# Kernel optimization log

Hardware: AMD Instinct MI355X
Metric: run time of the kernel (lower is better)

## Reference

```python
import jax, jax.numpy as jnp
import numpy as np

D_MODEL, H, D_K, D_V = 1024, 16, 64, 64
B, N = 8, 1024
EPS = 1e-9

def _xavier(key, shape):
    fan_in, fan_out = shape[1], shape[0]
    limit = float(np.sqrt(6.0 / (fan_in + fan_out)))
    return jax.random.uniform(key, shape, jnp.float32, -limit, limit)

def setup_inputs() -> dict:
    key = jax.random.key(0)
    ks = jax.random.split(key, 9)
    return {
        "queries": jax.random.normal(ks[0], (B, N, D_MODEL), jnp.float32),
        "keys":    jax.random.normal(ks[1], (B, N, D_MODEL), jnp.float32),
        "values":  jax.random.normal(ks[2], (B, N, D_MODEL), jnp.float32),
        "Wq": _xavier(ks[3], (H * D_K, D_MODEL)), "bq": jnp.zeros((H * D_K,), jnp.float32),
        "Wk": _xavier(ks[4], (H * D_K, D_MODEL)), "bk": jnp.zeros((H * D_K,), jnp.float32),
        "Wv": _xavier(ks[5], (H * D_V, D_MODEL)), "bv": jnp.zeros((H * D_V,), jnp.float32),
        "Wo": _xavier(ks[6], (D_MODEL, H * D_V)), "bo": jnp.zeros((D_MODEL,), jnp.float32),
        "Wb": _xavier(ks[7], (D_MODEL, D_MODEL)),  # bilinear weight[0]
        "bb": jnp.zeros((1,), jnp.float32),
        "lambda_param": jnp.asarray(1.0, jnp.float32),
    }

def reference(queries, keys, values, Wq, bq, Wk, bk, Wv, bv, Wo, bo, Wb, bb, lambda_param):
    b_s, nq, _ = queries.shape
    nk = keys.shape[1]
    # QKV projections -> [b, h, n, d]
    q = (queries @ Wq.T + bq).reshape(b_s, nq, H, D_K).transpose(0, 2, 1, 3)
    k = (keys    @ Wk.T + bk).reshape(b_s, nk, H, D_K).transpose(0, 2, 1, 3)
    v = (values  @ Wv.T + bv).reshape(b_s, nk, H, D_V).transpose(0, 2, 1, 3)
    att = jnp.einsum('bhqd,bhkd->bhqk', q, k) / jnp.sqrt(jnp.float32(D_K))
    # Phrasal scores: sigmoid(x W x^T + b), shape [b, nq, nq]
    xW = queries @ Wb  # [b, nq, d_model]
    P = jax.nn.sigmoid(jnp.einsum('bqd,bkd->bqk', xW, queries) + bb[0])
    att = att + lambda_param * jnp.log(P + EPS)[:, None, :, :]
    att = jax.nn.softmax(att, axis=-1)
    out = jnp.einsum('bhqk,bhkd->bhqd', att, v).transpose(0, 2, 1, 3).reshape(b_s, nq, H * D_V)
    out = out @ Wo.T + bo
    return (out, att, P)
```

## Files before the change

### kernel.cpp

```cpp
#include <hip/hip_runtime.h>
#include <cmath>


typedef _Float16 f16;
typedef _Float16 f16x8 __attribute__((ext_vector_type(8)));
typedef _Float16 f16x4 __attribute__((ext_vector_type(4)));
typedef float    f32x4 __attribute__((ext_vector_type(4)));

#define DEVI __device__ __forceinline__

DEVI void async16(const void* g, void* l) {
    __builtin_amdgcn_global_load_lds((const __attribute__((address_space(1))) unsigned int*)g,
                                     (__attribute__((address_space(3))) unsigned int*)l,
                                     16, 0, 0);
}


__global__ __launch_bounds__(256) void cast_qkv(
        const float* __restrict__ q, const float* __restrict__ k, const float* __restrict__ v,
        f16* __restrict__ qh, f16* __restrict__ ql, f16* __restrict__ kh, f16* __restrict__ vh)
{
    size_t i = ((size_t)blockIdx.x * 256 + threadIdx.x) * 4;
    f32x4 qv = *(const f32x4*)(q + i);
    f32x4 kv = *(const f32x4*)(k + i);
    f32x4 vv = *(const f32x4*)(v + i);
    f16x4 a, b, c, d;
#pragma unroll
    for (int j = 0; j < 4; ++j) {
        f16 h = (f16)qv[j];
        a[j] = h;
        b[j] = (f16)(qv[j] - (float)h);
        c[j] = (f16)kv[j];
        d[j] = (f16)vv[j];
    }
    *(f16x4*)(qh + i) = a;
    *(f16x4*)(ql + i) = b;
    *(f16x4*)(kh + i) = c;
    *(f16x4*)(vh + i) = d;
}

__global__ __launch_bounds__(256) void cast_w(
        const float* __restrict__ w0, const float* __restrict__ w1,
        const float* __restrict__ w2, const float* __restrict__ w3,
        f16* __restrict__ o0, f16* __restrict__ o1, f16* __restrict__ o2, f16* __restrict__ o3)
{
    size_t i = ((size_t)blockIdx.x * 256 + threadIdx.x) * 4;
    f32x4 a = *(const f32x4*)(w0 + i);
    f32x4 b = *(const f32x4*)(w1 + i);
    f32x4 c = *(const f32x4*)(w2 + i);
    f32x4 d = *(const f32x4*)(w3 + i);
    f16x4 ra, rb, rc, rd;
#pragma unroll
    for (int j = 0; j < 4; ++j) { ra[j] = (f16)a[j]; rb[j] = (f16)b[j]; rc[j] = (f16)c[j]; rd[j] = (f16)d[j]; }
    *(f16x4*)(o0 + i) = ra;
    *(f16x4*)(o1 + i) = rb;
    *(f16x4*)(o2 + i) = rc;
    *(f16x4*)(o3 + i) = rd;
}

__global__ __launch_bounds__(256) void wb_trans(const float* __restrict__ Wb,
                                                f16* __restrict__ Th, f16* __restrict__ Tl)
{
    __shared__ float tile[64][65];
    const int to = blockIdx.x, td = blockIdx.y, t = threadIdx.x;
#pragma unroll
    for (int it = 0; it < 16; ++it) {
        int e = it * 256 + t;
        int d = e >> 6, o = e & 63;
        tile[o][d] = Wb[(size_t)(td * 64 + d) * 1024 + to * 64 + o];
    }
    __syncthreads();
#pragma unroll
    for (int it = 0; it < 16; ++it) {
        int e = it * 256 + t;
        int o = e >> 6, d = e & 63;
        float v = tile[o][d];
        f16 h = (f16)v;
        size_t idx = (size_t)(to * 64 + o) * 1024 + td * 64 + d;
        Th[idx] = h;
        Tl[idx] = (f16)(v - (float)h);
    }
}

__global__ __launch_bounds__(256) void v_trans(const f16* __restrict__ Vb, f16* __restrict__ Vt)
{
    __shared__ f16 tile[64][72];
    const int nt = blockIdx.x, bh = blockIdx.y, t = threadIdx.x;
    const int b = bh >> 4, h = bh & 15;
#pragma unroll
    for (int it = 0; it < 16; ++it) {
        int e = it * 256 + t;
        int n = e >> 6, d = e & 63;
        tile[d][n] = Vb[((size_t)(b * 1024 + nt * 64 + n)) * 1024 + h * 64 + d];
    }
    __syncthreads();
#pragma unroll
    for (int it = 0; it < 16; ++it) {
        int e = it * 256 + t;
        int d = e >> 6, n = e & 63;
        Vt[((size_t)bh * 64 + d) * 1024 + nt * 64 + n] = tile[d][n];
    }
}

template<int MODE>
__global__ __launch_bounds__(256) void gemm_nt(
        const f16* __restrict__ A, const f16* __restrict__ B,
        const float* __restrict__ bias, void* __restrict__ Cout,
        int M, int N, int K, size_t sA, size_t sB, size_t sC)
{
    __shared__ __align__(16) f16 As[128 * 64];
    __shared__ __align__(16) f16 Bs[128 * 64];
    const int tid = threadIdx.x;
    const int lane = tid & 63;
    const int w = tid >> 6;
    const int wq = w >> 1, wn = w & 1;
    const int l15 = lane & 15, q4 = lane >> 4;
    const size_t z = blockIdx.z;
    const f16* Ab = A + z * sA;
    const f16* Bb = B + z * sB;
    const int tm = blockIdx.y * 128, tn = blockIdx.x * 128;
    const int srow = tid >> 3;
    const int scol = ((tid & 7) ^ (srow & 7)) << 3;

    f32x4 acc[4][4] = {};

    for (int k0 = 0; k0 < K; k0 += 64) {
#pragma unroll
        for (int c = 0; c < 4; ++c) {
            int r = (c << 5) + srow;
            async16(Ab + (size_t)(tm + r) * K + k0 + scol, &As[c * 2048 + tid * 8]);
            async16(Bb + (size_t)(tn + r) * K + k0 + scol, &Bs[c * 2048 + tid * 8]);
        }
        __syncthreads();
#pragma unroll
        for (int ks = 0; ks < 2; ++ks) {
            f16x8 af[4], bf[4];
#pragma unroll
            for (int i = 0; i < 4; ++i) {
                int m = wq * 64 + i * 16 + l15;
                af[i] = *(const f16x8*)&As[m * 64 + ((((ks << 2) + q4) ^ (m & 7)) << 3)];
                int n = wn * 64 + i * 16 + l15;
                bf[i] = *(const f16x8*)&Bs[n * 64 + ((((ks << 2) + q4) ^ (n & 7)) << 3)];
            }
#pragma unroll
            for (int mi = 0; mi < 4; ++mi)
#pragma unroll
                for (int ni = 0; ni < 4; ++ni)
                    acc[mi][ni] = __builtin_amdgcn_mfma_f32_16x16x32_f16(af[mi], bf[ni], acc[mi][ni], 0, 0, 0);
        }
        __syncthreads();
    }

#pragma unroll
    for (int mi = 0; mi < 4; ++mi)
#pragma unroll
        for (int ni = 0; ni < 4; ++ni) {
            const int col = tn + wn * 64 + ni * 16 + l15;
            const float bv = bias[col];
#pragma unroll
            for (int r = 0; r < 4; ++r) {
                const int row = tm + wq * 64 + mi * 16 + q4 * 4 + r;
                const float v = acc[mi][ni][r] + bv;
                const size_t idx = z * sC + (size_t)row * N + col;
                if (MODE == 0) ((float*)Cout)[idx] = v;
                else           ((f16*)Cout)[idx] = (f16)v;
            }
        }
}

template<int MODE>
__global__ __launch_bounds__(256) void gemm_nt3(
        const f16* __restrict__ Ah, const f16* __restrict__ Al,
        const f16* __restrict__ Bh, const f16* __restrict__ Bl,
        void* __restrict__ out0, void* __restrict__ out1,
        const float* __restrict__ bbp, const float* __restrict__ lamp,
        int M, int N, int K, size_t sA, size_t sB, size_t sC)
{
    __shared__ __align__(16) f16 Ash[128 * 32], Asl[128 * 32], Bsh[128 * 32], Bsl[128 * 32];
    const int tid = threadIdx.x;
    const int lane = tid & 63;
    const int w = tid >> 6;
    const int wq = w >> 1, wn = w & 1;
    const int l15 = lane & 15, q4 = lane >> 4;
    const size_t z = blockIdx.z;
    const f16* Ahb = Ah + z * sA; const f16* Alb = Al + z * sA;
    const f16* Bhb = Bh + z * sB; const f16* Blb = Bl + z * sB;
    const int tm = blockIdx.y * 128, tn = blockIdx.x * 128;
    const int srow = tid >> 2;
    const int scol = ((tid & 3) ^ (srow & 3)) << 3;

    f32x4 acc[4][4] = {};

    for (int k0 = 0; k0 < K; k0 += 32) {
#pragma unroll
        for (int c = 0; c < 2; ++c) {
            int r = (c << 6) + srow;
            const size_t ga = (size_t)(tm + r) * K + k0 + scol;
            const size_t gb = (size_t)(tn + r) * K + k0 + scol;
            async16(Ahb + ga, &Ash[c * 2048 + tid * 8]);
            async16(Alb + ga, &Asl[c * 2048 + tid * 8]);
            async16(Bhb + gb, &Bsh[c * 2048 + tid * 8]);
            async16(Blb + gb, &Bsl[c * 2048 + tid * 8]);
        }
        __syncthreads();
        f16x8 ah[4], al[4], bh[4], bl[4];
#pragma unroll
        for (int i = 0; i < 4; ++i) {
            int m = wq * 64 + i * 16 + l15;
            int offa = m * 32 + ((q4 ^ (m & 3)) << 3);
            ah[i] = *(const f16x8*)&Ash[offa];
            al[i] = *(const f16x8*)&Asl[offa];
            int n = wn * 64 + i * 16 + l15;
            int offb = n * 32 + ((q4 ^ (n & 3)) << 3);
            bh[i] = *(const f16x8*)&Bsh[offb];
            bl[i] = *(const f16x8*)&Bsl[offb];
        }
#pragma unroll
        for (int mi = 0; mi < 4; ++mi)
#pragma unroll
            for (int ni = 0; ni < 4; ++ni) {
                acc[mi][ni] = __builtin_amdgcn_mfma_f32_16x16x32_f16(ah[mi], bh[ni], acc[mi][ni], 0, 0, 0);
                acc[mi][ni] = __builtin_amdgcn_mfma_f32_16x16x32_f16(ah[mi], bl[ni], acc[mi][ni], 0, 0, 0);
                acc[mi][ni] = __builtin_amdgcn_mfma_f32_16x16x32_f16(al[mi], bh[ni], acc[mi][ni], 0, 0, 0);
            }
        __syncthreads();
    }

    float bb0 = 0.f, l8 = 0.f;
    if constexpr (MODE == 1) { bb0 = bbp[0]; l8 = 8.f * lamp[0]; }
#pragma unroll
    for (int mi = 0; mi < 4; ++mi)
#pragma unroll
        for (int ni = 0; ni < 4; ++ni) {
            const int row0 = tm + wq * 64 + mi * 16 + q4 * 4;
            const int col = tn + wn * 64 + ni * 16 + l15;
            if constexpr (MODE == 0) {
#pragma unroll
                for (int r = 0; r < 4; ++r) {
                    const size_t idx = z * sC + (size_t)(row0 + r) * N + col;
                    float v = acc[mi][ni][r];
                    f16 hi = (f16)v;
                    ((f16*)out0)[idx] = hi;
                    ((f16*)out1)[idx] = (f16)(v - (float)hi);
                }
            } else {
                f32x4 lpv;
#pragma unroll
                for (int r = 0; r < 4; ++r) {
                    float zt = acc[mi][ni][r] + bb0;
                    zt = fminf(fmaxf(zt, -87.f), 87.f);
                    float Pv = 1.f / (1.f + expf(-zt));
                    ((float*)out0)[z * sC + (size_t)(row0 + r) * N + col] = Pv;
                    lpv[r] = l8 * logf(Pv + 1e-9f);
                }
                *(f32x4*)&((float*)out1)[z * sC + (size_t)(row0 >> 2) * 4096 + (size_t)col * 4] = lpv;
            }
        }
}

__global__ __launch_bounds__(256) void attn_pass1(
        const f16* __restrict__ Qf, const f16* __restrict__ Kf,
        const float* __restrict__ Lp, float* __restrict__ linv)
{
    __shared__ __align__(16) f16 Ks[2][128 * 64];

    const int qt = blockIdx.x, h = blockIdx.y, b = blockIdx.z;
    const int tid = threadIdx.x, lane = tid & 63, w = tid >> 6;
    const int l15 = lane & 15, q4 = lane >> 4;

    f16x8 aq[2][2];
    const size_t qbase = ((size_t)(b * 1024 + qt * 128 + w * 32)) * 1024 + h * 64;
#pragma unroll
    for (int mi = 0; mi < 2; ++mi)
#pragma unroll
        for (int ks = 0; ks < 2; ++ks)
            aq[mi][ks] = *(const f16x8*)&Qf[qbase + (size_t)(mi * 16 + l15) * 1024 + ks * 32 + q4 * 8];

    const size_t kgbase = ((size_t)b * 1024) * 1024 + h * 64;
    const int srow = tid >> 3;
    const int scol = ((tid & 7) ^ (srow & 7)) << 3;
    const size_t lpb = (size_t)b * 1048576 + (size_t)(qt * 32 + w * 8 + q4) * 4096;

    float lsum[8];
#pragma unroll
    for (int i = 0; i < 8; ++i) lsum[i] = 0.f;

#pragma unroll
    for (int c = 0; c < 4; ++c) {
        int r = (c << 5) + srow;
        async16(&Kf[kgbase + (size_t)r * 1024 + scol], &Ks[0][c * 2048 + tid * 8]);
    }
    __syncthreads();

    int cur = 0;
    for (int kt = 0; kt < 8; ++kt) {
        if (kt < 7) {
#pragma unroll
            for (int c = 0; c < 4; ++c) {
                int r = (c << 5) + srow;
                async16(&Kf[kgbase + (size_t)((kt + 1) * 128 + r) * 1024 + scol],
                        &Ks[cur ^ 1][c * 2048 + tid * 8]);
            }
        }
        f32x4 sc[2][8];
#pragma unroll
        for (int mi = 0; mi < 2; ++mi)
#pragma unroll
            for (int ni = 0; ni < 8; ++ni)
                sc[mi][ni] = *(const f32x4*)&Lp[lpb + (size_t)mi * 16384 +
                                                (size_t)(kt * 128 + ni * 16 + l15) * 4];
#pragma unroll
        for (int ks = 0; ks < 2; ++ks)
#pragma unroll
            for (int ni = 0; ni < 8; ++ni) {
                int n = ni * 16 + l15;
                f16x8 bf = *(const f16x8*)&Ks[cur][n * 64 + ((((ks << 2) + q4) ^ (n & 7)) << 3)];
#pragma unroll
                for (int mi = 0; mi < 2; ++mi)
                    sc[mi][ni] = __builtin_amdgcn_mfma_f32_16x16x32_f16(aq[mi][ks], bf, sc[mi][ni], 0, 0, 0);
            }
#pragma unroll
        for (int mi = 0; mi < 2; ++mi)
#pragma unroll
            for (int r2 = 0; r2 < 4; ++r2) {
                float s = 0.f;
#pragma unroll
                for (int ni = 0; ni < 8; ++ni) s += __expf(sc[mi][ni][r2] * 0.125f);
                lsum[mi * 4 + r2] += s;
            }
        __syncthreads();
        cur ^= 1;
    }

#pragma unroll
    for (int i = 0; i < 8; ++i) {
        float s = lsum[i];
        s += __shfl_xor(s, 1, 16);
        s += __shfl_xor(s, 2, 16);
        s += __shfl_xor(s, 4, 16);
        s += __shfl_xor(s, 8, 16);
        lsum[i] = s;
    }
    if (l15 == 0) {
        const size_t ob = ((size_t)(b * 16 + h)) * 1024 + qt * 128 + w * 32;
#pragma unroll
        for (int mi = 0; mi < 2; ++mi)
#pragma unroll
            for (int r2 = 0; r2 < 4; ++r2)
                linv[ob + mi * 16 + q4 * 4 + r2] = 1.f / lsum[mi * 4 + r2];
    }
}

__global__ __launch_bounds__(256) void attn_pass2(
        const f16* __restrict__ Qf, const f16* __restrict__ Kf,
        const f16* __restrict__ Vt, const float* __restrict__ Lp,
        const float* __restrict__ linv,
        float* __restrict__ att, f16* __restrict__ Obf)
{
    __shared__ __align__(16) f16 Ks[128 * 64];
    __shared__ __align__(16) f16 Vs[64 * 128];
    __shared__ __align__(16) f16 atts[4][32 * 32];

    const int qt = blockIdx.x, h = blockIdx.y, b = blockIdx.z;
    const int tid = threadIdx.x, lane = tid & 63, w = tid >> 6;
    const int l15 = lane & 15, q4 = lane >> 4;

    f16x8 aq[2][2];
    const size_t qbase = ((size_t)(b * 1024 + qt * 128 + w * 32)) * 1024 + h * 64;
#pragma unroll
    for (int mi = 0; mi < 2; ++mi)
#pragma unroll
        for (int ks = 0; ks < 2; ++ks)
            aq[mi][ks] = *(const f16x8*)&Qf[qbase + (size_t)(mi * 16 + l15) * 1024 + ks * 32 + q4 * 8];

    float inv_l[8];
    {
        const size_t lb = ((size_t)(b * 16 + h)) * 1024 + qt * 128 + w * 32;
        f32x4 iv0 = *(const f32x4*)&linv[lb + q4 * 4];
        f32x4 iv1 = *(const f32x4*)&linv[lb + 16 + q4 * 4];
#pragma unroll
        for (int r = 0; r < 4; ++r) { inv_l[r] = iv0[r]; inv_l[4 + r] = iv1[r]; }
    }

    const size_t kgbase = ((size_t)b * 1024) * 1024 + h * 64;
    const size_t lpb = (size_t)b * 1048576 + (size_t)(qt * 32 + w * 8 + q4) * 4096;
    const size_t attbase = ((size_t)((b * 16 + h) * 1024 + qt * 128 + w * 32)) * 1024;
    const int srow = tid >> 3;
    const int scol = ((tid & 7) ^ (srow & 7)) << 3;
    const int vr0 = tid >> 4;
    const int vcb = ((tid & 15) ^ vr0) << 3;

    f32x4 oacc[2][4] = {};
    f16* atts_w = &atts[w][0];

    for (int kt = 0; kt < 8; ++kt) {
#pragma unroll
        for (int c = 0; c < 4; ++c) {
            int r = (c << 5) + srow;
            async16(&Kf[kgbase + (size_t)(kt * 128 + r) * 1024 + scol], &Ks[c * 2048 + tid * 8]);
            int vr = (c << 4) + vr0;
            async16(&Vt[((size_t)(b * 16 + h) * 64 + vr) * 1024 + kt * 128 + vcb], &Vs[c * 2048 + tid * 8]);
        }
        __syncthreads();
#pragma unroll
        for (int qx = 0; qx < 4; ++qx) {
            f32x4 sc[2][2];
#pragma unroll
            for (int mi = 0; mi < 2; ++mi)
#pragma unroll
                for (int nq = 0; nq < 2; ++nq)
                    sc[mi][nq] = *(const f32x4*)&Lp[lpb + (size_t)mi * 16384 +
                                  (size_t)(kt * 128 + qx * 32 + nq * 16 + l15) * 4];
#pragma unroll
            for (int ks = 0; ks < 2; ++ks)
#pragma unroll
                for (int nq = 0; nq < 2; ++nq) {
                    int n = qx * 32 + nq * 16 + l15;
                    f16x8 bf = *(const f16x8*)&Ks[n * 64 + ((((ks << 2) + q4) ^ (n & 7)) << 3)];
#pragma unroll
                    for (int mi = 0; mi < 2; ++mi)
                        sc[mi][nq] = __builtin_amdgcn_mfma_f32_16x16x32_f16(aq[mi][ks], bf, sc[mi][nq], 0, 0, 0);
                }
#pragma unroll
            for (int mi = 0; mi < 2; ++mi)
#pragma unroll
                for (int r2 = 0; r2 < 4; ++r2) {
                    const int ri = mi * 4 + r2;
                    const int qrl = mi * 16 + q4 * 4 + r2;
                    float* attq = &att[attbase + (size_t)qrl * 1024 + kt * 128 + qx * 32];
#pragma unroll
                    for (int nq = 0; nq < 2; ++nq) {
                        const int lc = nq * 16 + l15;
                        float a = __expf(sc[mi][nq][r2] * 0.125f) * inv_l[ri];
                        attq[lc] = a;
                        atts_w[qrl * 32 + (((lc >> 3) ^ ((qrl >> 1) & 3)) << 3) + (lc & 7)] = (f16)a;
                    }
                }
            f16x8 av[2];
#pragma unroll
            for (int mi = 0; mi < 2; ++mi) {
                int m = mi * 16 + l15;
                av[mi] = *(const f16x8*)&atts_w[m * 32 + ((q4 ^ ((m >> 1) & 3)) << 3)];
            }
#pragma unroll
            for (int nv = 0; nv < 4; ++nv) {
                int n = nv * 16 + l15;
                f16x8 bv = *(const f16x8*)&Vs[n * 128 + (((qx * 4 + q4) ^ (n & 15)) << 3)];
#pragma unroll
                for (int mi = 0; mi < 2; ++mi)
                    oacc[mi][nv] = __builtin_amdgcn_mfma_f32_16x16x32_f16(av[mi], bv, oacc[mi][nv], 0, 0, 0);
            }
        }
        __syncthreads();
    }

#pragma unroll
    for (int mi = 0; mi < 2; ++mi)
#pragma unroll
        for (int nv = 0; nv < 4; ++nv)
#pragma unroll
            for (int r2 = 0; r2 < 4; ++r2) {
                const size_t row = (size_t)(b * 1024 + qt * 128 + w * 32 + mi * 16 + q4 * 4 + r2);
                Obf[row * 1024 + h * 64 + nv * 16 + l15] = (f16)oacc[mi][nv][r2];
            }
}


extern "C" void kernel_launch(void* const* d_in, const int* in_sizes, int n_in,
                              void* d_out, int out_size, void* d_ws, size_t ws_size,
                              hipStream_t stream)
{
    (void)in_sizes; (void)n_in; (void)out_size; (void)ws_size;

    const float* queries = (const float*)d_in[0];
    const float* keys    = (const float*)d_in[1];
    const float* values  = (const float*)d_in[2];
    const float* Wq = (const float*)d_in[3];
    const float* bq = (const float*)d_in[4];
    const float* Wk = (const float*)d_in[5];
    const float* bk = (const float*)d_in[6];
    const float* Wv = (const float*)d_in[7];
    const float* bv = (const float*)d_in[8];
    const float* Wo = (const float*)d_in[9];
    const float* bo = (const float*)d_in[10];
    const float* Wb = (const float*)d_in[11];
    const float* bb = (const float*)d_in[12];
    const float* lam = (const float*)d_in[13];

    float* out  = (float*)d_out;
    float* attO = out + (size_t)8 * 1024 * 1024;
    float* POut = attO + (size_t)8 * 16 * 1024 * 1024;

    char* ws = (char*)d_ws;
    const size_t MB = 1024 * 1024;
    f16*  q_hi = (f16*)(ws + 0 * MB);
    f16*  q_lo = (f16*)(ws + 16 * MB);
    f16*  k_h  = (f16*)(ws + 32 * MB);
    f16*  v_h  = (f16*)(ws + 48 * MB);
    f16*  Qb   = (f16*)(ws + 64 * MB);
    f16*  Kb   = (f16*)(ws + 80 * MB);
    f16*  Vt   = (f16*)(ws + 96 * MB);
    float* Lp  = (float*)(ws + 112 * MB);
    f16*  Vb   = (f16*)(ws + 112 * MB);
    f16*  cWq  = (f16*)(ws + 144 * MB);
    f16*  cWk  = cWq + 1024 * 1024;
    f16*  cWv  = cWk + 1024 * 1024;
    f16*  cWo  = cWv + 1024 * 1024;
    f16*  Wbt_h = cWo + 1024 * 1024;
    f16*  Wbt_l = Wbt_h + 1024 * 1024;
    f16*  xw_h = k_h;
    f16*  xw_l = v_h;
    f16*  Obf  = q_lo;
    float* linv = (float*)q_hi;

    const size_t S1M = (size_t)1024 * 1024;

    cast_qkv<<<8192, 256, 0, stream>>>(queries, keys, values, q_hi, q_lo, k_h, v_h);
    cast_w<<<1024, 256, 0, stream>>>(Wq, Wk, Wv, Wo, cWq, cWk, cWv, cWo);
    wb_trans<<<dim3(16, 16), 256, 0, stream>>>(Wb, Wbt_h, Wbt_l);

    gemm_nt<1><<<dim3(8, 64), 256, 0, stream>>>(q_hi, cWq, bq, Qb, 8192, 1024, 1024, 0, 0, 0);
    gemm_nt<1><<<dim3(8, 64), 256, 0, stream>>>(k_h,  cWk, bk, Kb, 8192, 1024, 1024, 0, 0, 0);
    gemm_nt<1><<<dim3(8, 64), 256, 0, stream>>>(v_h,  cWv, bv, Vb, 8192, 1024, 1024, 0, 0, 0);
    v_trans<<<dim3(16, 128), 256, 0, stream>>>(Vb, Vt);

    gemm_nt3<0><<<dim3(8, 64), 256, 0, stream>>>(q_hi, q_lo, Wbt_h, Wbt_l,
                                                 xw_h, xw_l, nullptr, nullptr,
                                                 8192, 1024, 1024, 0, 0, 0);
    gemm_nt3<1><<<dim3(8, 8, 8), 256, 0, stream>>>(xw_h, xw_l, q_hi, q_lo,
                                                   POut, Lp, bb, lam,
                                                   1024, 1024, 1024, S1M, S1M, S1M);

    attn_pass1<<<dim3(8, 16, 8), 256, 0, stream>>>(Qb, Kb, Lp, linv);
    attn_pass2<<<dim3(8, 16, 8), 256, 0, stream>>>(Qb, Kb, Vt, Lp, linv, attO, Obf);

    gemm_nt<0><<<dim3(8, 64), 256, 0, stream>>>(Obf, cWo, bo, out, 8192, 1024, 1024, 0, 0, 0);
}
```

Baseline: 1.119 ms.

## Restructure split-precision GEMMs into segmented passes and tune attention exponentials

The three-term hi/lo split GEMM (hi*hi + hi*lo + lo*hi) is reorganised into three sequential K segments, each streaming one A/B pair through a single 64-wide LDS tile. This halves LDS traffic per step and uses a wider XOR swizzle. The sigmoid and log now use fast intrinsics. The attention passes switch to exp2 with a prescaled constant, and the 1/l normaliser is folded into the exponent as a log2 offset. s_setprio is raised around the MFMA blocks to favour matrix issue. The fast math approximations and the log2 fold can slightly change numerical accuracy.

```diff
diff --git a/kernel.cpp b/kernel.cpp
--- a/kernel.cpp
+++ b/kernel.cpp
@@ -8,6 +8,8 @@
 typedef float    f32x4 __attribute__((ext_vector_type(4)));
 
 #define DEVI __device__ __forceinline__
+
+#define C_EXP2 0.18033688011112042f
 
 DEVI void async16(const void* g, void* l) {
     __builtin_amdgcn_global_load_lds((const __attribute__((address_space(1))) unsigned int*)g,
@@ -169,61 +171,58 @@
 }
 
 template<int MODE>
-__global__ __launch_bounds__(256) void gemm_nt3(
-        const f16* __restrict__ Ah, const f16* __restrict__ Al,
-        const f16* __restrict__ Bh, const f16* __restrict__ Bl,
+__global__ __launch_bounds__(256) void gemm_ntseg(
+        const f16* __restrict__ A0, const f16* __restrict__ A1, const f16* __restrict__ A2,
+        const f16* __restrict__ B0, const f16* __restrict__ B1, const f16* __restrict__ B2,
         void* __restrict__ out0, void* __restrict__ out1,
         const float* __restrict__ bbp, const float* __restrict__ lamp,
-        int M, int N, int K, size_t sA, size_t sB, size_t sC)
-{
-    __shared__ __align__(16) f16 Ash[128 * 32], Asl[128 * 32], Bsh[128 * 32], Bsl[128 * 32];
+        int N, size_t sA, size_t sB, size_t sC)
+{
+    __shared__ __align__(16) f16 As[128 * 64];
+    __shared__ __align__(16) f16 Bs[128 * 64];
     const int tid = threadIdx.x;
     const int lane = tid & 63;
     const int w = tid >> 6;
     const int wq = w >> 1, wn = w & 1;
     const int l15 = lane & 15, q4 = lane >> 4;
     const size_t z = blockIdx.z;
-    const f16* Ahb = Ah + z * sA; const f16* Alb = Al + z * sA;
-    const f16* Bhb = Bh + z * sB; const f16* Blb = Bl + z * sB;
     const int tm = blockIdx.y * 128, tn = blockIdx.x * 128;
-    const int srow = tid >> 2;
-    const int scol = ((tid & 3) ^ (srow & 3)) << 3;
+    const int srow = tid >> 3;
+    const int scol = ((tid & 7) ^ (srow & 7)) << 3;
 
     f32x4 acc[4][4] = {};
 
-    for (int k0 = 0; k0 < K; k0 += 32) {
-#pragma unroll
-        for (int c = 0; c < 2; ++c) {
-            int r = (c << 6) + srow;
-            const size_t ga = (size_t)(tm + r) * K + k0 + scol;
-            const size_t gb = (size_t)(tn + r) * K + k0 + scol;
-            async16(Ahb + ga, &Ash[c * 2048 + tid * 8]);
-            async16(Alb + ga, &Asl[c * 2048 + tid * 8]);
-            async16(Bhb + gb, &Bsh[c * 2048 + tid * 8]);
-            async16(Blb + gb, &Bsl[c * 2048 + tid * 8]);
-        }
-        __syncthreads();
-        f16x8 ah[4], al[4], bh[4], bl[4];
-#pragma unroll
-        for (int i = 0; i < 4; ++i) {
-            int m = wq * 64 + i * 16 + l15;
-            int offa = m * 32 + ((q4 ^ (m & 3)) << 3);
-            ah[i] = *(const f16x8*)&Ash[offa];
-            al[i] = *(const f16x8*)&Asl[offa];
-            int n = wn * 64 + i * 16 + l15;
-            int offb = n * 32 + ((q4 ^ (n & 3)) << 3);
-            bh[i] = *(const f16x8*)&Bsh[offb];
-            bl[i] = *(const f16x8*)&Bsl[offb];
-        }
-#pragma unroll
-        for (int mi = 0; mi < 4; ++mi)
-#pragma unroll
-            for (int ni = 0; ni < 4; ++ni) {
-                acc[mi][ni] = __builtin_amdgcn_mfma_f32_16x16x32_f16(ah[mi], bh[ni], acc[mi][ni], 0, 0, 0);
-                acc[mi][ni] = __builtin_amdgcn_mfma_f32_16x16x32_f16(ah[mi], bl[ni], acc[mi][ni], 0, 0, 0);
-                acc[mi][ni] = __builtin_amdgcn_mfma_f32_16x16x32_f16(al[mi], bh[ni], acc[mi][ni], 0, 0, 0);
-            }
-        __syncthreads();
+#pragma unroll 1
+    for (int seg = 0; seg < 3; ++seg) {
+        const f16* Ab = (seg == 0 ? A0 : (seg == 1 ? A1 : A2)) + z * sA;
+        const f16* Bb = (seg == 0 ? B0 : (seg == 1 ? B1 : B2)) + z * sB;
+#pragma unroll 1
+        for (int k0 = 0; k0 < 1024; k0 += 64) {
+#pragma unroll
+            for (int c = 0; c < 4; ++c) {
+                int r = (c << 5) + srow;
+                async16(Ab + (size_t)(tm + r) * 1024 + k0 + scol, &As[c * 2048 + tid * 8]);
+                async16(Bb + (size_t)(tn + r) * 1024 + k0 + scol, &Bs[c * 2048 + tid * 8]);
+            }
+            __syncthreads();
+#pragma unroll
+            for (int ks = 0; ks < 2; ++ks) {
+                f16x8 af[4], bf[4];
+#pragma unroll
+                for (int i = 0; i < 4; ++i) {
+                    int m = wq * 64 + i * 16 + l15;
+                    af[i] = *(const f16x8*)&As[m * 64 + ((((ks << 2) + q4) ^ (m & 7)) << 3)];
+                    int n = wn * 64 + i * 16 + l15;
+                    bf[i] = *(const f16x8*)&Bs[n * 64 + ((((ks << 2) + q4) ^ (n & 7)) << 3)];
+                }
+#pragma unroll
+                for (int mi = 0; mi < 4; ++mi)
+#pragma unroll
+                    for (int ni = 0; ni < 4; ++ni)
+                        acc[mi][ni] = __builtin_amdgcn_mfma_f32_16x16x32_f16(af[mi], bf[ni], acc[mi][ni], 0, 0, 0);
+            }
+            __syncthreads();
+        }
     }
 
     float bb0 = 0.f, l8 = 0.f;
@@ -249,9 +248,9 @@
                 for (int r = 0; r < 4; ++r) {
                     float zt = acc[mi][ni][r] + bb0;
                     zt = fminf(fmaxf(zt, -87.f), 87.f);
-                    float Pv = 1.f / (1.f + expf(-zt));
+                    float Pv = 1.f / (1.f + __expf(-zt));
                     ((float*)out0)[z * sC + (size_t)(row0 + r) * N + col] = Pv;
-                    lpv[r] = l8 * logf(Pv + 1e-9f);
+                    lpv[r] = l8 * __logf(Pv + 1e-9f);
                 }
                 *(f32x4*)&((float*)out1)[z * sC + (size_t)(row0 >> 2) * 4096 + (size_t)col * 4] = lpv;
             }
@@ -309,6 +308,7 @@
             for (int ni = 0; ni < 8; ++ni)
                 sc[mi][ni] = *(const f32x4*)&Lp[lpb + (size_t)mi * 16384 +
                                                 (size_t)(kt * 128 + ni * 16 + l15) * 4];
+        __builtin_amdgcn_s_setprio(1);
 #pragma unroll
         for (int ks = 0; ks < 2; ++ks)
 #pragma unroll
@@ -319,13 +319,14 @@
                 for (int mi = 0; mi < 2; ++mi)
                     sc[mi][ni] = __builtin_amdgcn_mfma_f32_16x16x32_f16(aq[mi][ks], bf, sc[mi][ni], 0, 0, 0);
             }
+        __builtin_amdgcn_s_setprio(0);
 #pragma unroll
         for (int mi = 0; mi < 2; ++mi)
 #pragma unroll
             for (int r2 = 0; r2 < 4; ++r2) {
                 float s = 0.f;
 #pragma unroll
-                for (int ni = 0; ni < 8; ++ni) s += __expf(sc[mi][ni][r2] * 0.125f);
+                for (int ni = 0; ni < 8; ++ni) s += exp2f(sc[mi][ni][r2] * C_EXP2);
                 lsum[mi * 4 + r2] += s;
             }
         __syncthreads();
@@ -373,13 +374,15 @@
         for (int ks = 0; ks < 2; ++ks)
             aq[mi][ks] = *(const f16x8*)&Qf[qbase + (size_t)(mi * 16 + l15) * 1024 + ks * 32 + q4 * 8];
 
-    float inv_l[8];
+    float inv_l[8], il2[8];
     {
         const size_t lb = ((size_t)(b * 16 + h)) * 1024 + qt * 128 + w * 32;
         f32x4 iv0 = *(const f32x4*)&linv[lb + q4 * 4];
         f32x4 iv1 = *(const f32x4*)&linv[lb + 16 + q4 * 4];
 #pragma unroll
         for (int r = 0; r < 4; ++r) { inv_l[r] = iv0[r]; inv_l[4 + r] = iv1[r]; }
+#pragma unroll
+        for (int r = 0; r < 8; ++r) il2[r] = __log2f(inv_l[r]);
     }
 
     const size_t kgbase = ((size_t)b * 1024) * 1024 + h * 64;
@@ -411,6 +414,7 @@
                 for (int nq = 0; nq < 2; ++nq)
                     sc[mi][nq] = *(const f32x4*)&Lp[lpb + (size_t)mi * 16384 +
                                   (size_t)(kt * 128 + qx * 32 + nq * 16 + l15) * 4];
+            __builtin_amdgcn_s_setprio(1);
 #pragma unroll
             for (int ks = 0; ks < 2; ++ks)
 #pragma unroll
@@ -421,6 +425,7 @@
                     for (int mi = 0; mi < 2; ++mi)
                         sc[mi][nq] = __builtin_amdgcn_mfma_f32_16x16x32_f16(aq[mi][ks], bf, sc[mi][nq], 0, 0, 0);
                 }
+            __builtin_amdgcn_s_setprio(0);
 #pragma unroll
             for (int mi = 0; mi < 2; ++mi)
 #pragma unroll
@@ -431,7 +436,7 @@
 #pragma unroll
                     for (int nq = 0; nq < 2; ++nq) {
                         const int lc = nq * 16 + l15;
-                        float a = __expf(sc[mi][nq][r2] * 0.125f) * inv_l[ri];
+                        float a = exp2f(fmaf(sc[mi][nq][r2], C_EXP2, il2[ri]));
                         attq[lc] = a;
                         atts_w[qrl * 32 + (((lc >> 3) ^ ((qrl >> 1) & 3)) << 3) + (lc & 7)] = (f16)a;
                     }
@@ -442,6 +447,7 @@
                 int m = mi * 16 + l15;
                 av[mi] = *(const f16x8*)&atts_w[m * 32 + ((q4 ^ ((m >> 1) & 3)) << 3)];
             }
+            __builtin_amdgcn_s_setprio(1);
 #pragma unroll
             for (int nv = 0; nv < 4; ++nv) {
                 int n = nv * 16 + l15;
@@ -450,6 +456,7 @@
                 for (int mi = 0; mi < 2; ++mi)
                     oacc[mi][nv] = __builtin_amdgcn_mfma_f32_16x16x32_f16(av[mi], bv, oacc[mi][nv], 0, 0, 0);
             }
+            __builtin_amdgcn_s_setprio(0);
         }
         __syncthreads();
     }
@@ -524,12 +531,14 @@
     gemm_nt<1><<<dim3(8, 64), 256, 0, stream>>>(v_h,  cWv, bv, Vb, 8192, 1024, 1024, 0, 0, 0);
     v_trans<<<dim3(16, 128), 256, 0, stream>>>(Vb, Vt);
 
-    gemm_nt3<0><<<dim3(8, 64), 256, 0, stream>>>(q_hi, q_lo, Wbt_h, Wbt_l,
-                                                 xw_h, xw_l, nullptr, nullptr,
-                                                 8192, 1024, 1024, 0, 0, 0);
-    gemm_nt3<1><<<dim3(8, 8, 8), 256, 0, stream>>>(xw_h, xw_l, q_hi, q_lo,
-                                                   POut, Lp, bb, lam,
-                                                   1024, 1024, 1024, S1M, S1M, S1M);
+    gemm_ntseg<0><<<dim3(8, 64), 256, 0, stream>>>(q_hi, q_hi, q_lo,
+                                                   Wbt_h, Wbt_l, Wbt_h,
+                                                   xw_h, xw_l, nullptr, nullptr,
+                                                   1024, 0, 0, 0);
+    gemm_ntseg<1><<<dim3(8, 8, 8), 256, 0, stream>>>(xw_h, xw_h, xw_l,
+                                                     q_hi, q_lo, q_hi,
+                                                     POut, Lp, bb, lam,
+                                                     1024, S1M, S1M, S1M);
 
     attn_pass1<<<dim3(8, 16, 8), 256, 0, stream>>>(Qb, Kb, Lp, linv);
     attn_pass2<<<dim3(8, 16, 8), 256, 0, stream>>>(Qb, Kb, Vt, Lp, linv, attO, Obf);
```

New measurement: 1.122 ms. About the same (+0.3%).
